# Kernel optimization log

Hardware: AMD Instinct MI355X
Metric: run time of the kernel (lower is better)

Reference implementation:

```python
import jax, jax.numpy as jnp
import numpy as np

WIN = 9
EPS = 1e-05


def _box3d(x, win=WIN):
    """Sum over a win^3 box (zero-padded), equivalent to conv3d with a ones kernel.
    Implemented as three separable 1D convolutions (exact same math, O(win)/voxel)."""
    pad = win // 2
    for axis in range(3):  # spatial axes D, H, W
        kshape = [1, 1, 1, 1, 1]
        kshape[2 + axis] = win
        kern = jnp.ones(kshape, x.dtype)
        pads = [(0, 0)] * 3
        pads[axis] = (pad, pad)
        dn = jax.lax.conv_dimension_numbers(x.shape, kern.shape, ('NCDHW', 'OIDHW', 'NCDHW'))
        x = jax.lax.conv_general_dilated(x, kern, window_strides=(1, 1, 1),
                                         padding=pads, dimension_numbers=dn)
    return x


def setup_inputs() -> dict:
    key = jax.random.key(0)
    k1, k2 = jax.random.split(key)
    shape = (1, 1, 160, 192, 224)  # [N, C, D, H, W] brain-MRI-scale volume
    I = jax.random.normal(k1, shape, dtype=jnp.float32)
    J = jax.random.normal(k2, shape, dtype=jnp.float32)
    return {"I": I, "J": J}


def reference(I, J):
    win_size = WIN ** 3
    I2 = I * I
    J2 = J * J
    IJ = I * J
    I_sum = _box3d(I)
    J_sum = _box3d(J)
    I2_sum = _box3d(I2)
    J2_sum = _box3d(J2)
    IJ_sum = _box3d(IJ)
    u_I = I_sum / win_size
    u_J = J_sum / win_size
    cross = IJ_sum - u_J * I_sum - u_I * J_sum + u_I * u_J * win_size
    I_var = I2_sum - 2 * u_I * I_sum + u_I * u_I * win_size
    J_var = J2_sum - 2 * u_J * J_sum + u_J * u_J * win_size
    cc = cross * cross / (I_var * J_var + EPS)
    return -1.0 * jnp.mean(cc)
```

## Files before the change

### kernel.cpp

```cpp
#include <hip/hip_runtime.h>


#define DD 160
#define HH 192
#define WW 224
#define W4 56
#define SLICE (HH * WW)
#define S4 (SLICE / 4)
#define NVOX (DD * SLICE)
#define TW 32
#define TH 8
#define DCH 28
#define ITERS (DCH + 8)
#define NTHR 256
#define SW_RS 36
#define SW_CS (16 * SW_RS)
#define SH_SZ (TH * TW * 5)
#define EPS 1e-5f
#define INV_WSUM (1.0f / 729.0f)

__device__ __forceinline__ void bar_lds_only() {
    __asm__ volatile("" ::: "memory");
    __builtin_amdgcn_s_waitcnt(0xC07F);
    __builtin_amdgcn_s_barrier();
    __asm__ volatile("" ::: "memory");
}

__global__ __launch_bounds__(NTHR, 4) void ncc_fused(const float* __restrict__ I,
                                                     const float* __restrict__ J,
                                                     float* __restrict__ out) {
    __shared__ float SW[5 * SW_CS];
    __shared__ float SH0[SH_SZ], SH1[SH_SZ];
    __shared__ float wred[NTHR / 64];

    const int tid = threadIdx.x;
    const int tx = tid & 31, ty = tid >> 5;
    const int wlo = blockIdx.x * TW;
    const int hlo = blockIdx.y * TH;
    const int dlo = blockIdx.z * DCH;

    const int wid = tid - 128;
    const int wr = wid >> 3, wc = wid & 7;
    const int gh = hlo - 4 + wr;
    const bool hok = (gh >= 0) && (gh < HH);
    const int gf0 = (wlo >> 2) - 1 + wc;

    const int hcol = tid & 31, hch = tid >> 5;

    const float4* Iv = (const float4*)I;
    const float4* Jv = (const float4*)J;

    float pfa[12], pfb[12];

    auto w_load = [&](int z) {
        const bool zok = (z >= 0) && (z < DD) && hok;
        const int rowb = z * S4 + gh * W4;
        #pragma unroll
        for (int k = 0; k < 3; ++k) {
            const int f = gf0 + k;
            float4 a = make_float4(0.f, 0.f, 0.f, 0.f);
            float4 b = make_float4(0.f, 0.f, 0.f, 0.f);
            if (zok && f >= 0 && f < W4) { a = Iv[rowb + f]; b = Jv[rowb + f]; }
            pfa[4*k] = a.x; pfa[4*k+1] = a.y; pfa[4*k+2] = a.z; pfa[4*k+3] = a.w;
            pfb[4*k] = b.x; pfb[4*k+1] = b.y; pfb[4*k+2] = b.z; pfb[4*k+3] = b.w;
        }
    };

    auto w_compute = [&]() {
        float* wp = SW + wr * SW_RS + 4 * wc;
        #pragma unroll
        for (int ch = 0; ch < 5; ++ch) {
            float v[12];
            #pragma unroll
            for (int k = 0; k < 12; ++k)
                v[k] = (ch == 0) ? pfa[k]
                     : (ch == 1) ? pfb[k]
                     : (ch == 2) ? pfa[k] * pfa[k]
                     : (ch == 3) ? pfb[k] * pfb[k]
                     :             pfa[k] * pfb[k];
            float s = v[0];
            #pragma unroll
            for (int k = 1; k < 9; ++k) s += v[k];
            float4 o;
            o.x = s;
            s += v[9]  - v[0]; o.y = s;
            s += v[10] - v[1]; o.z = s;
            s += v[11] - v[2]; o.w = s;
            *(float4*)(wp + ch * SW_CS) = o;
        }
    };

    float q0[9], q1[9], q2[9], q3[9], q4[9];
    #pragma unroll
    for (int k = 0; k < 9; ++k) { q0[k]=0.f; q1[k]=0.f; q2[k]=0.f; q3[k]=0.f; q4[k]=0.f; }
    float r0=0.f, r1=0.f, r2=0.f, r3=0.f, r4=0.f;
    float acc = 0.f;

    if (tid >= 128) {
        w_load(dlo - 4);
        if (dlo >= 4) w_compute();
        w_load(dlo - 3);
    }
    bar_lds_only();

    #pragma unroll 1
    for (int g = 0; g < 4; ++g) {
        #pragma unroll
        for (int ph = 0; ph < 9; ++ph) {
            const int i = 9 * g + ph;
            const int z = dlo - 4 + i;
            const bool val = (z >= 0) && (z < DD);
            float* shW = (i & 1) ? SH1 : SH0;

            if (tid < 160 && val) {
                const float* p = SW + hch * SW_CS + hcol;
                float v[16];
                #pragma unroll
                for (int r = 0; r < 16; r += 2) {
                    const float* pr = p + r * SW_RS;
                    v[r]     = pr[0];
                    v[r + 1] = pr[SW_RS];
                }
                float s = v[0];
                #pragma unroll
                for (int r = 1; r < 9; ++r) s += v[r];
                float* o = shW + hcol * 5 + hch;
                float prev = s;
                o[0] = s;
                #pragma unroll
                for (int r = 1; r < TH; ++r) {
                    prev += v[r + 8] - v[r - 1];
                    o[r * (TW * 5)] = prev;
                }
            }
            bar_lds_only();

            float w0=0.f, w1=0.f, w2=0.f, w3=0.f, w4=0.f;
            if (val) {
                const float* pF = shW + (ty * TW + tx) * 5;
                w0 = pF[0]; w1 = pF[1]; w2 = pF[2]; w3 = pF[3]; w4 = pF[4];
            }
            if (tid >= 128 && i < ITERS - 1) {
                const int zn = z + 1;
                if (zn >= 0 && zn < DD) w_compute();
                w_load(z + 2);
            }
            r0 += w0 - q0[ph]; q0[ph] = w0;
            r1 += w1 - q1[ph]; q1[ph] = w1;
            r2 += w2 - q2[ph]; q2[ph] = w2;
            r3 += w3 - q3[ph]; q3[ph] = w3;
            r4 += w4 - q4[ph]; q4[ph] = w4;

            if (i >= 8 && (dlo + i - 8) < DD) {
                float cross = r4 - r0 * r1 * INV_WSUM;
                float iv    = r2 - r0 * r0 * INV_WSUM;
                float jv    = r3 - r1 * r1 * INV_WSUM;
                acc += cross * cross * __builtin_amdgcn_rcpf(iv * jv + EPS);
            }
            bar_lds_only();
        }
    }

    #pragma unroll
    for (int off = 32; off > 0; off >>= 1) acc += __shfl_down(acc, off, 64);
    if ((tid & 63) == 0) wred[tid >> 6] = acc;
    __syncthreads();
    if (tid == 0) {
        float t = 0.f;
        #pragma unroll
        for (int k = 0; k < NTHR / 64; ++k) t += wred[k];
        atomicAdd(out, t * (-1.0f / (float)NVOX));
    }
}

extern "C" void kernel_launch(void* const* d_in, const int* in_sizes, int n_in,
                              void* d_out, int out_size, void* d_ws, size_t ws_size,
                              hipStream_t stream) {
    const float* I = (const float*)d_in[0];
    const float* J = (const float*)d_in[1];
    float* out = (float*)d_out;

    hipMemsetAsync(d_out, 0, sizeof(float), stream);

    dim3 blk(NTHR, 1, 1);
    dim3 grd(WW / TW, HH / TH, (DD + DCH - 1) / DCH);
    ncc_fused<<<grd, blk, 0, stream>>>(I, J, out);
}
```

Measured before the change: 127.6 us.

## Software-pipeline W and H box-sum stages with double-buffered LDS, one barrier per slice

```diff
diff --git a/kernel.cpp b/kernel.cpp
--- a/kernel.cpp
+++ b/kernel.cpp
@@ -29,7 +29,7 @@
 __global__ __launch_bounds__(NTHR, 4) void ncc_fused(const float* __restrict__ I,
                                                      const float* __restrict__ J,
                                                      float* __restrict__ out) {
-    __shared__ float SW[5 * SW_CS];
+    __shared__ float SW0[5 * SW_CS], SW1[5 * SW_CS];
     __shared__ float SH0[SH_SZ], SH1[SH_SZ];
     __shared__ float wred[NTHR / 64];
 
@@ -66,8 +66,8 @@
         }
     };
 
-    auto w_compute = [&]() {
-        float* wp = SW + wr * SW_RS + 4 * wc;
+    auto w_compute = [&](float* dst) {
+        float* wp = dst + wr * SW_RS + 4 * wc;
         #pragma unroll
         for (int ch = 0; ch < 5; ++ch) {
             float v[12];
@@ -90,74 +90,89 @@
         }
     };
 
+    auto h_phase = [&](const float* swSrc, float* shDst) {
+        const float* p = swSrc + hch * SW_CS + hcol;
+        float v[16];
+        #pragma unroll
+        for (int r = 0; r < 16; r += 2) {
+            const float* pr = p + r * SW_RS;
+            v[r]     = pr[0];
+            v[r + 1] = pr[SW_RS];
+        }
+        float s = v[0];
+        #pragma unroll
+        for (int r = 1; r < 9; ++r) s += v[r];
+        float* o = shDst + hcol * 5 + hch;
+        float prev = s;
+        o[0] = s;
+        #pragma unroll
+        for (int r = 1; r < TH; ++r) {
+            prev += v[r + 8] - v[r - 1];
+            o[r * (TW * 5)] = prev;
+        }
+    };
+
     float q0[9], q1[9], q2[9], q3[9], q4[9];
     #pragma unroll
     for (int k = 0; k < 9; ++k) { q0[k]=0.f; q1[k]=0.f; q2[k]=0.f; q3[k]=0.f; q4[k]=0.f; }
     float r0=0.f, r1=0.f, r2=0.f, r3=0.f, r4=0.f;
     float acc = 0.f;
 
+    const int z0 = dlo - 4;
     if (tid >= 128) {
-        w_load(dlo - 4);
-        if (dlo >= 4) w_compute();
-        w_load(dlo - 3);
+        w_load(z0);
+        if (z0 >= 0) w_compute(SW0);
+        w_load(z0 + 1);
     }
     bar_lds_only();
+
+    if (tid < 160 && z0 >= 0) h_phase(SW0, SH0);
+    if (tid >= 128) {
+        const int z1 = z0 + 1;
+        if (z1 >= 0 && z1 < DD) w_compute(SW1);
+        w_load(z0 + 2);
+    }
 
     #pragma unroll 1
     for (int g = 0; g < 4; ++g) {
         #pragma unroll
         for (int ph = 0; ph < 9; ++ph) {
-            const int i = 9 * g + ph;
-            const int z = dlo - 4 + i;
+            const int j = 9 * g + ph;
+            const int z = dlo - 4 + j;
+            bar_lds_only();
+
             const bool val = (z >= 0) && (z < DD);
-            float* shW = (i & 1) ? SH1 : SH0;
-
-            if (tid < 160 && val) {
-                const float* p = SW + hch * SW_CS + hcol;
-                float v[16];
-                #pragma unroll
-                for (int r = 0; r < 16; r += 2) {
-                    const float* pr = p + r * SW_RS;
-                    v[r]     = pr[0];
-                    v[r + 1] = pr[SW_RS];
-                }
-                float s = v[0];
-                #pragma unroll
-                for (int r = 1; r < 9; ++r) s += v[r];
-                float* o = shW + hcol * 5 + hch;
-                float prev = s;
-                o[0] = s;
-                #pragma unroll
-                for (int r = 1; r < TH; ++r) {
-                    prev += v[r + 8] - v[r - 1];
-                    o[r * (TW * 5)] = prev;
-                }
-            }
-            bar_lds_only();
-
+            float* shR = (j & 1) ? SH1 : SH0;
             float w0=0.f, w1=0.f, w2=0.f, w3=0.f, w4=0.f;
             if (val) {
-                const float* pF = shW + (ty * TW + tx) * 5;
+                const float* pF = shR + (ty * TW + tx) * 5;
                 w0 = pF[0]; w1 = pF[1]; w2 = pF[2]; w3 = pF[3]; w4 = pF[4];
             }
-            if (tid >= 128 && i < ITERS - 1) {
-                const int zn = z + 1;
-                if (zn >= 0 && zn < DD) w_compute();
-                w_load(z + 2);
-            }
+
+            if ((g < 3 || ph < 8) && tid < 160) {
+                const int zh = z + 1;
+                if (zh >= 0 && zh < DD)
+                    h_phase((j & 1) ? SW0 : SW1, (j & 1) ? SH0 : SH1);
+            }
+
+            if ((g < 3 || ph < 7) && tid >= 128) {
+                const int zw = z + 2;
+                if (zw >= 0 && zw < DD) w_compute((j & 1) ? SW1 : SW0);
+                w_load(z + 3);
+            }
+
             r0 += w0 - q0[ph]; q0[ph] = w0;
             r1 += w1 - q1[ph]; q1[ph] = w1;
             r2 += w2 - q2[ph]; q2[ph] = w2;
             r3 += w3 - q3[ph]; q3[ph] = w3;
             r4 += w4 - q4[ph]; q4[ph] = w4;
 
-            if (i >= 8 && (dlo + i - 8) < DD) {
+            if (j >= 8 && (dlo + j - 8) < DD) {
                 float cross = r4 - r0 * r1 * INV_WSUM;
                 float iv    = r2 - r0 * r0 * INV_WSUM;
                 float jv    = r3 - r1 * r1 * INV_WSUM;
                 acc += cross * cross * __builtin_amdgcn_rcpf(iv * jv + EPS);
             }
-            bar_lds_only();
         }
     }
 
```

After: 126.0 us. About the same (-1.2%).
